# Performance work log

Hardware: AMD Instinct MI355X
Metric: run time of the kernel (lower is better)

## Reference

```python
import jax, jax.numpy as jnp
import numpy as np

N = 50000        # atoms
NEIGH = 12       # neighbors per atom
HID = 128
B = 500          # crystals (100 atoms each, contiguous)
NCLS = 2
BSTEPS, BMIN, BMAX = 40, 0.0, 8.0
ASTEPS, AMIN, AMAX = 10, -1.0, 1.0


def gbf(d, dmin, dmax, steps):
    # Gaussian basis expansion: exp(-(d - mu)^2 / gamma^2)
    filters = jnp.linspace(dmin, dmax, steps)
    gamma = (dmax - dmin) / steps
    return jnp.exp(-(d[..., None] - filters) ** 2 / gamma ** 2)


def sage_conv(x, W_l, b_l, W_r, dst, n):
    # PyG SAGEConv (mean aggr): out[d] = lin_l(mean_{src->d} x[src]) + lin_r(x[d])
    # lin commutes with mean, so project first (N x HID) to avoid a 600k x F gather.
    h = x @ W_l.T                                  # [N, HID]
    h_src = jnp.repeat(h, NEIGH, axis=0)           # source of edge e = e // NEIGH
    s = jax.ops.segment_sum(h_src, dst, num_segments=n)
    cnt = jax.ops.segment_sum(jnp.ones(dst.shape, h.dtype), dst, num_segments=n)
    agg = s / jnp.maximum(cnt, 1.0)[:, None]
    return agg + b_l + x @ W_r.T


def setup_inputs() -> dict:
    key = jax.random.key(0)
    ks = jax.random.split(key, 20)
    inp = {
        "bond_fea": jax.random.uniform(ks[0], (N, NEIGH), jnp.float32) * 8.0,
        "angle_fea": jax.random.uniform(ks[1], (N, NEIGH, NEIGH), jnp.float32) * 2.0 - 1.0,
        "species": jax.random.randint(ks[2], (N,), 0, 100),
        "nbr_idx": jax.random.randint(ks[3], (N, NEIGH), 0, N),
        "crys_idx": jnp.stack([jnp.arange(B) * 100, (jnp.arange(B) + 1) * 100], axis=1),
    }
    def w(k, shape):
        return jax.random.normal(k, shape, jnp.float32) * 0.05
    inp.update({
        "W1b": w(ks[4], (HID, BSTEPS * NEIGH)), "b1b": jnp.zeros((HID,), jnp.float32),
        "W1br": w(ks[5], (HID, BSTEPS * NEIGH)),
        "W1a": w(ks[6], (HID, ASTEPS * NEIGH * NEIGH)), "b1a": jnp.zeros((HID,), jnp.float32),
        "W1ar": w(ks[7], (HID, ASTEPS * NEIGH * NEIGH)),
        "W2b": w(ks[8], (HID, HID)), "b2b": jnp.zeros((HID,), jnp.float32),
        "W2br": w(ks[9], (HID, HID)),
        "W2a": w(ks[10], (HID, HID)), "b2a": jnp.zeros((HID,), jnp.float32),
        "W2ar": w(ks[11], (HID, HID)),
        "Wfc": w(ks[12], (NCLS, 2 * HID)), "bfc": jnp.zeros((NCLS,), jnp.float32),
    })
    return inp


def reference(bond_fea, angle_fea, W1b, b1b, W1br, W1a, b1a, W1ar,
              W2b, b2b, W2br, W2a, b2a, W2ar, Wfc, bfc,
              species, nbr_idx, crys_idx):
    dst = nbr_idx.reshape(-1)                               # [N*NEIGH]
    edge_fea = gbf(bond_fea, BMIN, BMAX, BSTEPS).reshape(N, -1)    # [N, 480]
    angle_f = gbf(angle_fea, AMIN, AMAX, ASTEPS).reshape(N, -1)    # [N, 1440]

    bo = jax.nn.relu(sage_conv(edge_fea, W1b, b1b, W1br, dst, N))
    ao = jax.nn.relu(sage_conv(angle_f, W1a, b1a, W1ar, dst, N))
    # dropout omitted (deterministic eval-mode reference)
    bo = jax.nn.relu(sage_conv(bo, W2b, b2b, W2br, dst, N))
    ao = jax.nn.relu(sage_conv(ao, W2a, b2a, W2ar, dst, N))

    crys_fea = jnp.concatenate([bo, ao], axis=1)            # [N, 256]
    # segment-mean pooling over contiguous [start, end) crystal ranges
    seg = jnp.searchsorted(crys_idx[:, 1], jnp.arange(N), side="right")
    cnt = (crys_idx[:, 1] - crys_idx[:, 0]).astype(crys_fea.dtype)
    pooled = jax.ops.segment_sum(crys_fea, seg, num_segments=B) / cnt[:, None]
    return pooled @ Wfc.T + bfc
```

## Files before the change

### kernel.cpp

```cpp
#include <hip/hip_runtime.h>

#define NEIGHB 12
#define HIDD 128
#define CAP 40

typedef _Float16 half8 __attribute__((ext_vector_type(8)));
typedef float f32x4 __attribute__((ext_vector_type(4)));

__global__ __launch_bounds__(256) void cvt_pack(
    const float* __restrict__ W1b, const float* __restrict__ W1br, _Float16* __restrict__ O1b,
    const float* __restrict__ W1a, const float* __restrict__ W1ar, _Float16* __restrict__ O1a,
    const float* __restrict__ W2b, const float* __restrict__ W2br, _Float16* __restrict__ O2b,
    const float* __restrict__ W2a, const float* __restrict__ W2ar, _Float16* __restrict__ O2a) {
    int blk = blockIdx.x;
    const float *Wl, *Wr; _Float16* out; int K, Kp, base;
    if (blk < 512)       { Wl = W1b; Wr = W1br; out = O1b; K = 480;  Kp = 512;  base = 0; }
    else if (blk < 1984) { Wl = W1a; Wr = W1ar; out = O1a; K = 1440; Kp = 1472; base = 512; }
    else if (blk < 2112) { Wl = W2b; Wr = W2br; out = O2b; K = 128;  Kp = 128;  base = 1984; }
    else                 { Wl = W2a; Wr = W2ar; out = O2a; K = 128;  Kp = 128;  base = 2112; }
    int idx = (blk - base) * 256 + threadIdx.x;
    int n = idx / Kp, k = idx - n * Kp;
    float v = 0.f;
    if (k < K) v = (n < HIDD) ? Wl[(size_t)n * K + k] : Wr[(size_t)(n - HIDD) * K + k];
    int t = k >> 6, s = (k >> 5) & 1, g = (k >> 3) & 3, e = k & 7;
    int nb = n >> 4, col = n & 15;
    size_t addr = ((((size_t)t * 16 + nb) * 2 + s) * 64 + (g * 16 + col)) * 8 + e;
    out[addr] = (_Float16)v;
}

template <int MODE, int KTOT, int KP>
__device__ __forceinline__ void gemm_body(
    const void* __restrict__ Ain, const _Float16* __restrict__ Wp,
    _Float16* __restrict__ Cl, _Float16* __restrict__ Cr,
    int rows, int mb, _Float16* As) {
    constexpr int SUB  = (MODE == 2) ? 10 : 40;
    constexpr int RAWC = (MODE == 2) ? 144 : 12;
    constexpr float MU0 = (MODE == 2) ? -1.0f : 0.0f;
    constexpr float DMU = (MODE == 2) ? (2.0f / 9.0f) : (8.0f / 39.0f);
    constexpr int NT = KP / 64;

    const int tid = threadIdx.x;
    const int lane = tid & 63;
    const int wave = tid >> 6;
    const int iBase = mb * 64;
    const int mrow = tid >> 3;
    const int g = tid & 7;
    const int g8 = g * 8;

    const int gi0 = min(iBase + mrow, rows - 1);
    const int gi1 = min(iBase + mrow + 32, rows - 1);
    const _Float16* Ap = (const _Float16*)Ain;
    const float* rr0 = (const float*)Ain + (size_t)gi0 * RAWC;
    const float* rr1 = (const float*)Ain + (size_t)gi1 * RAWC;

    half8 bA[8], bB[8], aExp[2];
    float r0v[2], r1v[2];

#define PREFB(T, DST)                                                             \
    {                                                                             \
        _Pragma("unroll")                                                         \
        for (int q = 0; q < 8; ++q) {                                             \
            int s_ = q >> 2, b_ = q & 3;                                          \
            (DST)[q] = *reinterpret_cast<const half8*>(                           \
                Wp + ((((size_t)(T) * 16 + (wave * 4 + b_)) * 2 + s_) * 64 + lane) * 8); \
        }                                                                         \
    }

#define LOADA(T)                                                                  \
    {                                                                             \
        if (MODE == 0) {                                                          \
            aExp[0] = *reinterpret_cast<const half8*>(Ap + (size_t)gi0 * KP + (T) * 64 + g8); \
            aExp[1] = *reinterpret_cast<const half8*>(Ap + (size_t)gi1 * KP + (T) * 64 + g8); \
        } else {                                                                  \
            int k0 = (T) * 64 + g8;                                               \
            if (k0 < KTOT) {                                                      \
                int j0 = k0 / SUB;                                                \
                r0v[0] = rr0[j0]; r0v[1] = rr1[j0];                               \
                if (MODE == 2) {                                                  \
                    int jn = min(j0 + 1, RAWC - 1);                               \
                    r1v[0] = rr0[jn]; r1v[1] = rr1[jn];                           \
                }                                                                 \
            }                                                                     \
        }                                                                         \
    }

#define EXPAND(T)                                                                 \
    if (MODE != 0) {                                                              \
        int k0 = (T) * 64 + g8;                                                   \
        if (k0 < KTOT) {                                                          \
            int j0 = k0 / SUB, t0 = k0 - j0 * SUB;                                \
            _Pragma("unroll")                                                     \
            for (int q = 0; q < 2; ++q) {                                         \
                float ra = r0v[q];                                                \
                float rb = (MODE == 2) ? r1v[q] : r0v[q];                         \
                half8 v;                                                          \
                _Pragma("unroll")                                                 \
                for (int e2 = 0; e2 < 8; ++e2) {                                  \
                    int tt = t0 + e2;                                             \
                    bool c2 = (tt >= SUB);                                        \
                    float dd = (c2 ? rb : ra) -                                   \
                               (MU0 + (float)(c2 ? tt - SUB : tt) * DMU);         \
                    v[e2] = (_Float16)__expf(-25.f * dd * dd);                    \
                }                                                                 \
                aExp[q] = v;                                                      \
            }                                                                     \
        } else {                                                                  \
            _Pragma("unroll")                                                     \
            for (int q = 0; q < 2; ++q) {                                         \
                half8 v;                                                          \
                _Pragma("unroll")                                                 \
                for (int e2 = 0; e2 < 8; ++e2) v[e2] = (_Float16)0.f;             \
                aExp[q] = v;                                                      \
            }                                                                     \
        }                                                                         \
    }

#define WRAS(BUF)                                                                 \
    {                                                                             \
        _Pragma("unroll")                                                         \
        for (int q = 0; q < 2; ++q) {                                             \
            int m_ = mrow + 32 * q;                                               \
            *reinterpret_cast<half8*>(As + (BUF) * 4096 + m_ * 64 +               \
                                      ((g ^ (m_ & 7)) << 3)) = aExp[q];           \
        }                                                                         \
    }

#define COMPUTE(BUF, BREG)                                                        \
    {                                                                             \
        _Pragma("unroll")                                                         \
        for (int s_ = 0; s_ < 2; ++s_) {                                          \
            int cg = s_ * 4 + (lane >> 4);                                        \
            half8 af[4];                                                          \
            _Pragma("unroll")                                                     \
            for (int a_ = 0; a_ < 4; ++a_) {                                      \
                int m_ = a_ * 16 + (lane & 15);                                   \
                af[a_] = *reinterpret_cast<const half8*>(                         \
                    As + (BUF) * 4096 + m_ * 64 + ((cg ^ (m_ & 7)) << 3));        \
            }                                                                     \
            _Pragma("unroll")                                                     \
            for (int a_ = 0; a_ < 4; ++a_)                                        \
                _Pragma("unroll")                                                 \
                for (int b_ = 0; b_ < 4; ++b_)                                    \
                    acc[a_][b_] = __builtin_amdgcn_mfma_f32_16x16x32_f16(         \
                        af[a_], (BREG)[s_ * 4 + b_], acc[a_][b_], 0, 0, 0);       \
        }                                                                         \
    }

#define STEP(T, BCUR, BNEXT)                                                      \
    {                                                                             \
        __syncthreads();                                                          \
        const bool hn = (T) + 1 < NT;                                             \
        if (hn) { PREFB((T) + 1, BNEXT); LOADA((T) + 1); }                        \
        COMPUTE((T) & 1, BCUR);                                                   \
        if (hn) { EXPAND((T) + 1); WRAS(((T) + 1) & 1); }                         \
    }

    f32x4 acc[4][4];
#pragma unroll
    for (int a = 0; a < 4; ++a)
#pragma unroll
        for (int b = 0; b < 4; ++b)
#pragma unroll
            for (int r = 0; r < 4; ++r) acc[a][b][r] = 0.f;

    PREFB(0, bA);
    LOADA(0);
    EXPAND(0);
    WRAS(0);

#pragma unroll 1
    for (int t = 0; t < NT; t += 2) {
        STEP(t, bA, bB);
        if (t + 1 < NT) STEP(t + 1, bB, bA);
    }
#undef PREFB
#undef LOADA
#undef EXPAND
#undef WRAS
#undef COMPUTE
#undef STEP

    _Float16* Cout = (wave < 2) ? Cl : Cr;
    int nBase = (wave & 1) * 64;
#pragma unroll
    for (int a = 0; a < 4; ++a) {
        int mrel = a * 16 + ((lane >> 4) << 2);
#pragma unroll
        for (int r = 0; r < 4; ++r) {
            int m = iBase + mrel + r;
            if (m < rows) {
#pragma unroll
                for (int b = 0; b < 4; ++b) {
                    int n = nBase + b * 16 + (lane & 15);
                    Cout[(size_t)m * HIDD + n] = (_Float16)acc[a][b][r];
                }
            }
        }
    }
}

__global__ __launch_bounds__(256) void gemm_l1(
    const float* __restrict__ bond, const _Float16* __restrict__ Wb,
    _Float16* __restrict__ Hbl, _Float16* __restrict__ Hbr,
    const float* __restrict__ angle, const _Float16* __restrict__ Wa,
    _Float16* __restrict__ Hal, _Float16* __restrict__ Har, int rows, int aGB) {
    __shared__ __align__(16) _Float16 As[2 * 64 * 64];
    if ((int)blockIdx.x < aGB)
        gemm_body<2, 1440, 1472>(angle, Wa, Hal, Har, rows, blockIdx.x, As);
    else
        gemm_body<1, 480, 512>(bond, Wb, Hbl, Hbr, rows, blockIdx.x - aGB, As);
}

__global__ __launch_bounds__(256) void gemm_l2(
    const _Float16* __restrict__ bo, const _Float16* __restrict__ Wb,
    _Float16* __restrict__ Hbl, _Float16* __restrict__ Hbr,
    const _Float16* __restrict__ ao, const _Float16* __restrict__ Wa,
    _Float16* __restrict__ Hal, _Float16* __restrict__ Har, int rows) {
    __shared__ __align__(16) _Float16 As[2 * 64 * 64];
    if (blockIdx.y == 0)
        gemm_body<0, 128, 128>(bo, Wb, Hbl, Hbr, rows, blockIdx.x, As);
    else
        gemm_body<0, 128, 128>(ao, Wa, Hal, Har, rows, blockIdx.x, As);
}

__global__ void build_inc(const int* __restrict__ nbr, int* __restrict__ cnt,
                          int* __restrict__ inc, int nEdges) {
    int e = blockIdx.x * blockDim.x + threadIdx.x;
    if (e >= nEdges) return;
    int d = nbr[e];
    int src = e / NEIGHB;
    int pos = atomicAdd(&cnt[d], 1);
    if (pos < CAP) inc[(size_t)d * CAP + pos] = src;
}

__global__ __launch_bounds__(256) void agg2(
    const _Float16* __restrict__ Hbl, const _Float16* __restrict__ Hbr,
    const _Float16* __restrict__ Hal, const _Float16* __restrict__ Har,
    const int* __restrict__ cnt, const int* __restrict__ inc,
    const float* __restrict__ biasB, const float* __restrict__ biasA,
    _Float16* __restrict__ Ob, _Float16* __restrict__ Oa, int N) {
    int d = blockIdx.x * 16 + (threadIdx.x >> 4);
    if (d >= N) return;
    int c8 = (threadIdx.x & 15) * 8;
    int c = cnt[d];
    int cc = min(c, CAP);
    const int* lst = inc + (size_t)d * CAP;
    int4 q0 = *reinterpret_cast<const int4*>(lst);
    int4 q1 = *reinterpret_cast<const int4*>(lst + 4);
    int4 q2 = *reinterpret_cast<const int4*>(lst + 8);
    int idx[12] = {q0.x, q0.y, q0.z, q0.w, q1.x, q1.y, q1.z, q1.w,
                   q2.x, q2.y, q2.z, q2.w};
    half8 vb[12], va[12];
#pragma unroll
    for (int e = 0; e < 12; ++e) {
        int ii = (e < cc) ? idx[e] : 0;
        vb[e] = *reinterpret_cast<const half8*>(Hbl + (size_t)ii * HIDD + c8);
        va[e] = *reinterpret_cast<const half8*>(Hal + (size_t)ii * HIDD + c8);
    }
    float sb[8], sa[8];
#pragma unroll
    for (int j = 0; j < 8; ++j) { sb[j] = 0.f; sa[j] = 0.f; }
#pragma unroll
    for (int e = 0; e < 12; ++e) {
        float w = (e < cc) ? 1.f : 0.f;
#pragma unroll
        for (int j = 0; j < 8; ++j) {
            sb[j] = fmaf(w, (float)vb[e][j], sb[j]);
            sa[j] = fmaf(w, (float)va[e][j], sa[j]);
        }
    }
    for (int e = 12; e < cc; ++e) {
        int ii = lst[e];
        half8 xb = *reinterpret_cast<const half8*>(Hbl + (size_t)ii * HIDD + c8);
        half8 xa = *reinterpret_cast<const half8*>(Hal + (size_t)ii * HIDD + c8);
#pragma unroll
        for (int j = 0; j < 8; ++j) { sb[j] += (float)xb[j]; sa[j] += (float)xa[j]; }
    }
    float inv = 1.f / (float)max(c, 1);
    half8 rb = *reinterpret_cast<const half8*>(Hbr + (size_t)d * HIDD + c8);
    half8 ra = *reinterpret_cast<const half8*>(Har + (size_t)d * HIDD + c8);
    float4 bb0 = *reinterpret_cast<const float4*>(biasB + c8);
    float4 bb1 = *reinterpret_cast<const float4*>(biasB + c8 + 4);
    float4 ba0 = *reinterpret_cast<const float4*>(biasA + c8);
    float4 ba1 = *reinterpret_cast<const float4*>(biasA + c8 + 4);
    float fb[8] = {bb0.x, bb0.y, bb0.z, bb0.w, bb1.x, bb1.y, bb1.z, bb1.w};
    float fa[8] = {ba0.x, ba0.y, ba0.z, ba0.w, ba1.x, ba1.y, ba1.z, ba1.w};
    half8 ob, oa;
#pragma unroll
    for (int j = 0; j < 8; ++j) {
        ob[j] = (_Float16)fmaxf(sb[j] * inv + fb[j] + (float)rb[j], 0.f);
        oa[j] = (_Float16)fmaxf(sa[j] * inv + fa[j] + (float)ra[j], 0.f);
    }
    *reinterpret_cast<half8*>(Ob + (size_t)d * HIDD + c8) = ob;
    *reinterpret_cast<half8*>(Oa + (size_t)d * HIDD + c8) = oa;
}

__global__ __launch_bounds__(256) void pool_fc(const _Float16* __restrict__ bo,
                                               const _Float16* __restrict__ ao,
                                               const int* __restrict__ crys,
                                               const float* __restrict__ Wfc,
                                               const float* __restrict__ bfc,
                                               float* __restrict__ out) {
    __shared__ float red0[256];
    __shared__ float red1[256];
    int b = blockIdx.x;
    int t = threadIdx.x;
    int s0 = crys[b * 2 + 0];
    int s1 = crys[b * 2 + 1];
    const _Float16* src = (t < HIDD) ? bo : ao;
    int col = t & (HIDD - 1);
    float s = 0.f;
    for (int i = s0; i < s1; ++i) s += (float)src[(size_t)i * HIDD + col];
    float pooled = s / (float)(s1 - s0);
    red0[t] = pooled * Wfc[t];
    red1[t] = pooled * Wfc[256 + t];
    __syncthreads();
    for (int off = 128; off >= 1; off >>= 1) {
        if (t < off) {
            red0[t] += red0[t + off];
            red1[t] += red1[t + off];
        }
        __syncthreads();
    }
    if (t == 0) {
        out[b * 2 + 0] = red0[0] + bfc[0];
        out[b * 2 + 1] = red1[0] + bfc[1];
    }
}

extern "C" void kernel_launch(void* const* d_in, const int* in_sizes, int n_in,
                              void* d_out, int out_size, void* d_ws, size_t ws_size,
                              hipStream_t stream) {
    const float* bond = (const float*)d_in[0];
    const float* angle = (const float*)d_in[1];
    const int* nbr = (const int*)d_in[3];
    const int* crys = (const int*)d_in[4];
    const float* W1b = (const float*)d_in[5];
    const float* b1b = (const float*)d_in[6];
    const float* W1br = (const float*)d_in[7];
    const float* W1a = (const float*)d_in[8];
    const float* b1a = (const float*)d_in[9];
    const float* W1ar = (const float*)d_in[10];
    const float* W2b = (const float*)d_in[11];
    const float* b2b = (const float*)d_in[12];
    const float* W2br = (const float*)d_in[13];
    const float* W2a = (const float*)d_in[14];
    const float* b2a = (const float*)d_in[15];
    const float* W2ar = (const float*)d_in[16];
    const float* Wfc = (const float*)d_in[17];
    const float* bfc = (const float*)d_in[18];
    float* out = (float*)d_out;

    const int N = in_sizes[2];
    const int B = in_sizes[4] / 2;
    const int nEdges = N * NEIGHB;

    char* p = (char*)d_ws;
    _Float16* Hbl = (_Float16*)p;  p += (size_t)N * HIDD * 2;
    _Float16* Hbr = (_Float16*)p;  p += (size_t)N * HIDD * 2;
    _Float16* Hal = (_Float16*)p;  p += (size_t)N * HIDD * 2;
    _Float16* Har = (_Float16*)p;  p += (size_t)N * HIDD * 2;
    _Float16* bo  = (_Float16*)p;  p += (size_t)N * HIDD * 2;
    _Float16* ao  = (_Float16*)p;  p += (size_t)N * HIDD * 2;
    _Float16* bo2 = (_Float16*)p;  p += (size_t)N * HIDD * 2;
    _Float16* ao2 = (_Float16*)p;  p += (size_t)N * HIDD * 2;
    int* cnt = (int*)p;            p += (size_t)N * 4;
    int* inc = (int*)p;            p += (size_t)N * CAP * 4;
    _Float16* W1bp = (_Float16*)p; p += 256 * 512 * 2;
    _Float16* W1ap = (_Float16*)p; p += 256 * 1472 * 2;
    _Float16* W2bp = (_Float16*)p; p += 256 * 128 * 2;
    _Float16* W2ap = (_Float16*)p;

    hipMemsetAsync(cnt, 0, (size_t)N * 4, stream);
    build_inc<<<(nEdges + 255) / 256, 256, 0, stream>>>(nbr, cnt, inc, nEdges);
    cvt_pack<<<2240, 256, 0, stream>>>(W1b, W1br, W1bp, W1a, W1ar, W1ap,
                                       W2b, W2br, W2bp, W2a, W2ar, W2ap);

    const int gB = (N + 63) / 64;
    const int aB = (N + 15) / 16;

    gemm_l1<<<gB * 2, 256, 0, stream>>>(bond, W1bp, Hbl, Hbr,
                                        angle, W1ap, Hal, Har, N, gB);
    agg2<<<aB, 256, 0, stream>>>(Hbl, Hbr, Hal, Har, cnt, inc, b1b, b1a, bo, ao, N);
    gemm_l2<<<dim3(gB, 2), 256, 0, stream>>>(bo, W2bp, Hbl, Hbr,
                                             ao, W2ap, Hal, Har, N);
    agg2<<<aB, 256, 0, stream>>>(Hbl, Hbr, Hal, Har, cnt, inc, b2b, b2a, bo2, ao2, N);

    pool_fc<<<B, 256, 0, stream>>>(bo2, ao2, crys, Wfc, bfc, out);
}
```

Before: 410.8 us.

## Use 512-thread persistent GEMM blocks with halved per-wave tiles and exp2

Rewrites the layer-1 and layer-2 projection GEMMs to use 512-thread blocks. Each of the 8 waves now computes a 64x32 output slice instead of 64x64, so accumulator and B-prefetch registers are halved and more waves can be resident. The kernels become persistent grid-stride loops over 512 blocks, and a barrier is added before the first shared-memory write so blocks can be reused across jobs. The Gaussian expansion now calls the hardware exp2 with a prescaled constant instead of __expf. The risk is that each wave does less MFMA work per B-fragment load, and the fixed grid of 512 may underfill the GPU or load-balance unevenly between angle and bond jobs.

```diff
diff --git a/kernel.cpp b/kernel.cpp
--- a/kernel.cpp
+++ b/kernel.cpp
@@ -29,7 +29,7 @@
 }
 
 template <int MODE, int KTOT, int KP>
-__device__ __forceinline__ void gemm_body(
+__device__ __forceinline__ void gemm_body512(
     const void* __restrict__ Ain, const _Float16* __restrict__ Wp,
     _Float16* __restrict__ Cl, _Float16* __restrict__ Cr,
     int rows, int mb, _Float16* As) {
@@ -37,49 +37,44 @@
     constexpr int RAWC = (MODE == 2) ? 144 : 12;
     constexpr float MU0 = (MODE == 2) ? -1.0f : 0.0f;
     constexpr float DMU = (MODE == 2) ? (2.0f / 9.0f) : (8.0f / 39.0f);
+    constexpr float NL2 = -36.067375f;
     constexpr int NT = KP / 64;
 
     const int tid = threadIdx.x;
     const int lane = tid & 63;
     const int wave = tid >> 6;
     const int iBase = mb * 64;
-    const int mrow = tid >> 3;
+    const int m = tid >> 3;
     const int g = tid & 7;
     const int g8 = g * 8;
 
-    const int gi0 = min(iBase + mrow, rows - 1);
-    const int gi1 = min(iBase + mrow + 32, rows - 1);
+    const int gi = min(iBase + m, rows - 1);
     const _Float16* Ap = (const _Float16*)Ain;
-    const float* rr0 = (const float*)Ain + (size_t)gi0 * RAWC;
-    const float* rr1 = (const float*)Ain + (size_t)gi1 * RAWC;
-
-    half8 bA[8], bB[8], aExp[2];
-    float r0v[2], r1v[2];
+    const float* rr = (const float*)Ain + (size_t)gi * RAWC;
+
+    half8 bA[4], bB[4], aExp;
+    float r0v, r1v;
 
 #define PREFB(T, DST)                                                             \
     {                                                                             \
         _Pragma("unroll")                                                         \
-        for (int q = 0; q < 8; ++q) {                                             \
-            int s_ = q >> 2, b_ = q & 3;                                          \
+        for (int q = 0; q < 4; ++q) {                                             \
+            int s_ = q >> 1, b_ = q & 1;                                          \
             (DST)[q] = *reinterpret_cast<const half8*>(                           \
-                Wp + ((((size_t)(T) * 16 + (wave * 4 + b_)) * 2 + s_) * 64 + lane) * 8); \
+                Wp + ((((size_t)(T) * 16 + (wave * 2 + b_)) * 2 + s_) * 64 + lane) * 8); \
         }                                                                         \
     }
 
 #define LOADA(T)                                                                  \
     {                                                                             \
         if (MODE == 0) {                                                          \
-            aExp[0] = *reinterpret_cast<const half8*>(Ap + (size_t)gi0 * KP + (T) * 64 + g8); \
-            aExp[1] = *reinterpret_cast<const half8*>(Ap + (size_t)gi1 * KP + (T) * 64 + g8); \
+            aExp = *reinterpret_cast<const half8*>(Ap + (size_t)gi * KP + (T) * 64 + g8); \
         } else {                                                                  \
             int k0 = (T) * 64 + g8;                                               \
             if (k0 < KTOT) {                                                      \
                 int j0 = k0 / SUB;                                                \
-                r0v[0] = rr0[j0]; r0v[1] = rr1[j0];                               \
-                if (MODE == 2) {                                                  \
-                    int jn = min(j0 + 1, RAWC - 1);                               \
-                    r1v[0] = rr0[jn]; r1v[1] = rr1[jn];                           \
-                }                                                                 \
+                r0v = rr[j0];                                                     \
+                if (MODE == 2) r1v = rr[min(j0 + 1, RAWC - 1)];                   \
             }                                                                     \
         }                                                                         \
     }
@@ -89,41 +84,24 @@
         int k0 = (T) * 64 + g8;                                                   \
         if (k0 < KTOT) {                                                          \
             int j0 = k0 / SUB, t0 = k0 - j0 * SUB;                                \
+            half8 v;                                                              \
             _Pragma("unroll")                                                     \
-            for (int q = 0; q < 2; ++q) {                                         \
-                float ra = r0v[q];                                                \
-                float rb = (MODE == 2) ? r1v[q] : r0v[q];                         \
-                half8 v;                                                          \
-                _Pragma("unroll")                                                 \
-                for (int e2 = 0; e2 < 8; ++e2) {                                  \
-                    int tt = t0 + e2;                                             \
-                    bool c2 = (tt >= SUB);                                        \
-                    float dd = (c2 ? rb : ra) -                                   \
-                               (MU0 + (float)(c2 ? tt - SUB : tt) * DMU);         \
-                    v[e2] = (_Float16)__expf(-25.f * dd * dd);                    \
-                }                                                                 \
-                aExp[q] = v;                                                      \
+            for (int e2 = 0; e2 < 8; ++e2) {                                      \
+                int tt = t0 + e2;                                                 \
+                bool c2 = (tt >= SUB);                                            \
+                float dd = ((MODE == 2 && c2) ? r1v : r0v) -                      \
+                           (MU0 + (float)(c2 ? tt - SUB : tt) * DMU);             \
+                v[e2] = (_Float16)__builtin_amdgcn_exp2f(NL2 * dd * dd);          \
             }                                                                     \
+            aExp = v;                                                             \
         } else {                                                                  \
             _Pragma("unroll")                                                     \
-            for (int q = 0; q < 2; ++q) {                                         \
-                half8 v;                                                          \
-                _Pragma("unroll")                                                 \
-                for (int e2 = 0; e2 < 8; ++e2) v[e2] = (_Float16)0.f;             \
-                aExp[q] = v;                                                      \
-            }                                                                     \
+            for (int e2 = 0; e2 < 8; ++e2) aExp[e2] = (_Float16)0.f;              \
         }                                                                         \
     }
 
 #define WRAS(BUF)                                                                 \
-    {                                                                             \
-        _Pragma("unroll")                                                         \
-        for (int q = 0; q < 2; ++q) {                                             \
-            int m_ = mrow + 32 * q;                                               \
-            *reinterpret_cast<half8*>(As + (BUF) * 4096 + m_ * 64 +               \
-                                      ((g ^ (m_ & 7)) << 3)) = aExp[q];           \
-        }                                                                         \
-    }
+    *reinterpret_cast<half8*>(As + (BUF) * 4096 + m * 64 + ((g ^ (m & 7)) << 3)) = aExp;
 
 #define COMPUTE(BUF, BREG)                                                        \
     {                                                                             \
@@ -140,9 +118,9 @@
             _Pragma("unroll")                                                     \
             for (int a_ = 0; a_ < 4; ++a_)                                        \
                 _Pragma("unroll")                                                 \
-                for (int b_ = 0; b_ < 4; ++b_)                                    \
+                for (int b_ = 0; b_ < 2; ++b_)                                    \
                     acc[a_][b_] = __builtin_amdgcn_mfma_f32_16x16x32_f16(         \
-                        af[a_], (BREG)[s_ * 4 + b_], acc[a_][b_], 0, 0, 0);       \
+                        af[a_], (BREG)[s_ * 2 + b_], acc[a_][b_], 0, 0, 0);       \
         }                                                                         \
     }
 
@@ -155,17 +133,18 @@
         if (hn) { EXPAND((T) + 1); WRAS(((T) + 1) & 1); }                         \
     }
 
-    f32x4 acc[4][4];
+    f32x4 acc[4][2];
 #pragma unroll
     for (int a = 0; a < 4; ++a)
 #pragma unroll
-        for (int b = 0; b < 4; ++b)
+        for (int b = 0; b < 2; ++b)
 #pragma unroll
             for (int r = 0; r < 4; ++r) acc[a][b][r] = 0.f;
 
     PREFB(0, bA);
     LOADA(0);
     EXPAND(0);
+    __syncthreads();
     WRAS(0);
 
 #pragma unroll 1
@@ -180,47 +159,53 @@
 #undef COMPUTE
 #undef STEP
 
-    _Float16* Cout = (wave < 2) ? Cl : Cr;
-    int nBase = (wave & 1) * 64;
+    _Float16* Cout = (wave < 4) ? Cl : Cr;
+    int nBase = (wave & 3) * 32;
 #pragma unroll
     for (int a = 0; a < 4; ++a) {
         int mrel = a * 16 + ((lane >> 4) << 2);
 #pragma unroll
         for (int r = 0; r < 4; ++r) {
-            int m = iBase + mrel + r;
-            if (m < rows) {
-#pragma unroll
-                for (int b = 0; b < 4; ++b) {
+            int mm = iBase + mrel + r;
+            if (mm < rows) {
+#pragma unroll
+                for (int b = 0; b < 2; ++b) {
                     int n = nBase + b * 16 + (lane & 15);
-                    Cout[(size_t)m * HIDD + n] = (_Float16)acc[a][b][r];
+                    Cout[(size_t)mm * HIDD + n] = (_Float16)acc[a][b][r];
                 }
             }
         }
     }
 }
 
-__global__ __launch_bounds__(256) void gemm_l1(
+__global__ __launch_bounds__(512, 4) void gemm_l1p(
     const float* __restrict__ bond, const _Float16* __restrict__ Wb,
     _Float16* __restrict__ Hbl, _Float16* __restrict__ Hbr,
     const float* __restrict__ angle, const _Float16* __restrict__ Wa,
-    _Float16* __restrict__ Hal, _Float16* __restrict__ Har, int rows, int aGB) {
-    __shared__ __align__(16) _Float16 As[2 * 64 * 64];
-    if ((int)blockIdx.x < aGB)
-        gemm_body<2, 1440, 1472>(angle, Wa, Hal, Har, rows, blockIdx.x, As);
-    else
-        gemm_body<1, 480, 512>(bond, Wb, Hbl, Hbr, rows, blockIdx.x - aGB, As);
-}
-
-__global__ __launch_bounds__(256) void gemm_l2(
+    _Float16* __restrict__ Hal, _Float16* __restrict__ Har,
+    int rows, int nA, int nTot) {
+    __shared__ __align__(16) _Float16 As[2 * 4096];
+    for (int job = blockIdx.x; job < nTot; job += gridDim.x) {
+        if (job < nA)
+            gemm_body512<2, 1440, 1472>(angle, Wa, Hal, Har, rows, job, As);
+        else
+            gemm_body512<1, 480, 512>(bond, Wb, Hbl, Hbr, rows, job - nA, As);
+    }
+}
+
+__global__ __launch_bounds__(512, 4) void gemm_l2p(
     const _Float16* __restrict__ bo, const _Float16* __restrict__ Wb,
     _Float16* __restrict__ Hbl, _Float16* __restrict__ Hbr,
     const _Float16* __restrict__ ao, const _Float16* __restrict__ Wa,
-    _Float16* __restrict__ Hal, _Float16* __restrict__ Har, int rows) {
-    __shared__ __align__(16) _Float16 As[2 * 64 * 64];
-    if (blockIdx.y == 0)
-        gemm_body<0, 128, 128>(bo, Wb, Hbl, Hbr, rows, blockIdx.x, As);
-    else
-        gemm_body<0, 128, 128>(ao, Wa, Hal, Har, rows, blockIdx.x, As);
+    _Float16* __restrict__ Hal, _Float16* __restrict__ Har,
+    int rows, int nA, int nTot) {
+    __shared__ __align__(16) _Float16 As[2 * 4096];
+    for (int job = blockIdx.x; job < nTot; job += gridDim.x) {
+        if (job < nA)
+            gemm_body512<0, 128, 128>(bo, Wb, Hbl, Hbr, rows, job, As);
+        else
+            gemm_body512<0, 128, 128>(ao, Wa, Hal, Har, rows, job - nA, As);
+    }
 }
 
 __global__ void build_inc(const int* __restrict__ nbr, int* __restrict__ cnt,
@@ -379,11 +364,11 @@
     const int gB = (N + 63) / 64;
     const int aB = (N + 15) / 16;
 
-    gemm_l1<<<gB * 2, 256, 0, stream>>>(bond, W1bp, Hbl, Hbr,
-                                        angle, W1ap, Hal, Har, N, gB);
+    gemm_l1p<<<512, 512, 0, stream>>>(bond, W1bp, Hbl, Hbr,
+                                      angle, W1ap, Hal, Har, N, gB, gB * 2);
     agg2<<<aB, 256, 0, stream>>>(Hbl, Hbr, Hal, Har, cnt, inc, b1b, b1a, bo, ao, N);
-    gemm_l2<<<dim3(gB, 2), 256, 0, stream>>>(bo, W2bp, Hbl, Hbr,
-                                             ao, W2ap, Hal, Har, N);
+    gemm_l2p<<<512, 512, 0, stream>>>(bo, W2bp, Hbl, Hbr,
+                                      ao, W2ap, Hal, Har, N, gB, gB * 2);
     agg2<<<aB, 256, 0, stream>>>(Hbl, Hbr, Hal, Har, cnt, inc, b2b, b2a, bo2, ao2, N);
 
     pool_fc<<<B, 256, 0, stream>>>(bo2, ao2, crys, Wfc, bfc, out);
```

After: 422.9 us. 1.03x slower.
